# Kernel optimization log

Hardware: AMD Instinct MI355X
Metric: run time of the kernel (lower is better)

The kernel has to match this reference:

```python
import jax, jax.numpy as jnp
import numpy as np

N_NODES = 100000
N_EDGES = 1200000
DIM = 64


def _gcn_layer(h, src, dst, norm, W, b):
    # GCNConv: linear -> gather -> normalize -> scatter-add -> bias
    n = h.shape[0]
    h = h @ W                              # [N, D]
    msg = h[src] * norm[:, None]           # [E+N, D] gathered edge messages
    out = jax.ops.segment_sum(msg, dst, num_segments=n)
    return out + b


def setup_inputs() -> dict:
    key = jax.random.key(0)
    ks = jax.random.split(key, 8)
    s = 1.0 / np.sqrt(DIM)
    return {
        "x": jax.random.normal(ks[0], (N_NODES, DIM), jnp.float32),
        "edge_index": jax.random.randint(ks[1], (2, N_EDGES), 0, N_NODES, dtype=jnp.int32),
        "W1": jax.random.normal(ks[2], (DIM, DIM), jnp.float32) * s,
        "b1": jnp.zeros((DIM,), jnp.float32),
        "W2": jax.random.normal(ks[3], (DIM, DIM), jnp.float32) * s,
        "b2": jnp.zeros((DIM,), jnp.float32),
        "W3": jax.random.normal(ks[4], (DIM, DIM), jnp.float32) * s,
        "b3": jnp.zeros((DIM,), jnp.float32),
    }


def reference(x, edge_index, W1, b1, W2, b2, W3, b3):
    n = x.shape[0]
    loops = jnp.arange(n, dtype=edge_index.dtype)
    src = jnp.concatenate([edge_index[0], loops])   # add self-loops (PyG GCNConv default)
    dst = jnp.concatenate([edge_index[1], loops])
    # symmetric degree normalization: norm_e = d^-1/2[src] * d^-1/2[dst]
    deg = jax.ops.segment_sum(jnp.ones(src.shape, x.dtype), dst, num_segments=n)
    dinv = jnp.where(deg > 0, jax.lax.rsqrt(deg), 0.0)
    norm = dinv[src] * dinv[dst]
    h = jax.nn.relu(_gcn_layer(x, src, dst, norm, W1, b1))   # dropout inactive at eval
    h = jax.nn.relu(_gcn_layer(h, src, dst, norm, W2, b2))
    return _gcn_layer(h, src, dst, norm, W3, b3)
```

## Files before the change

### kernel.cpp

```cpp
#include <hip/hip_runtime.h>
#include <math.h>

#define N_NODES 100000
#define N_EDGES 1200000
#define DIM 64
#define ELL_STRIDE 48
#define BNODES 128
#define NBUCKET ((N_NODES + BNODES - 1) / BNODES)
#define BIN_SHIFT 10
#define NBIN ((N_NODES + 1023) >> 10)
#define BIN_CAP 16384
#define CAP 40
#define BIN_BLOCKS 512
#define EPB ((N_EDGES + BIN_BLOCKS - 1) / BIN_BLOCKS)
#define GEMM_BLOCKS ((N_NODES + 63) / 64)
#define GW_BLOCKS (N_NODES / 16)

#define PACK(s, dloc) (((unsigned)(dloc) << 17) | (unsigned)(s))
#define UNPACK_S(p)   ((int)((p) & 0x1FFFF))
#define UNPACK_D(p)   ((int)((p) >> 17))

typedef __attribute__((ext_vector_type(8))) short bf16x8;
typedef __attribute__((ext_vector_type(4))) float f32x4;

__device__ __forceinline__ unsigned short f2bf(float f) {
    union { float f; unsigned int u; } v; v.f = f;
    unsigned int r = v.u + 0x7FFF + ((v.u >> 16) & 1);
    return (unsigned short)(r >> 16);
}
__device__ __forceinline__ float bf2f(unsigned short us) {
    return __uint_as_float((unsigned int)us << 16);
}

#define LDH(boff) bf2f(*(const unsigned short*)((const char*)h + ((unsigned)(boff) + bo)))


__global__ void k_init(int* __restrict__ tail) {
    if (threadIdx.x < NBIN) tail[threadIdx.x * 16] = 0;
}


__device__ __forceinline__ void gemm_block(int bid, const float* __restrict__ x,
                                           const float* __restrict__ W,
                                           unsigned short* __restrict__ h,
                                           float4* __restrict__ Xlds) {
    const int tid = threadIdx.x;
    const int lane = tid & 63;

    float wreg[64];
#pragma unroll
    for (int k = 0; k < 64; ++k) wreg[k] = W[k * DIM + lane];

    const int base = bid * 64;
#pragma unroll
    for (int it = 0; it < 4; ++it) {
        int f = tid + it * 256;
        int row = base + (f >> 4);
        if (row >= N_NODES) row = N_NODES - 1;
        Xlds[f] = ((const float4*)x)[row * 16 + (f & 15)];
    }
    __syncthreads();

    const int m0 = (tid >> 6) * 16;
    for (int m = 0; m < 16; ++m) {
        const float4* xr = &Xlds[(m0 + m) * 16];
        float a0 = 0.f, a1 = 0.f, a2 = 0.f, a3 = 0.f;
#pragma unroll
        for (int k4 = 0; k4 < 16; ++k4) {
            float4 xv = xr[k4];
            a0 = fmaf(xv.x, wreg[k4 * 4 + 0], a0);
            a1 = fmaf(xv.y, wreg[k4 * 4 + 1], a1);
            a2 = fmaf(xv.z, wreg[k4 * 4 + 2], a2);
            a3 = fmaf(xv.w, wreg[k4 * 4 + 3], a3);
        }
        int row = base + m0 + m;
        if (row < N_NODES)
            h[(size_t)row * DIM + lane] = f2bf((a0 + a1) + (a2 + a3));
    }
}


__global__ void __launch_bounds__(256) k_pre(const int* __restrict__ ei,
                                             const float* __restrict__ x,
                                             const float* __restrict__ W1,
                                             int* __restrict__ tail,
                                             unsigned* __restrict__ part,
                                             unsigned short* __restrict__ h) {
    __shared__ __align__(16) char smraw[16384];
    __shared__ int lcnt[NBIN];
    __shared__ int gbase[NBIN];
    __shared__ int gcnt[NBIN];

    if (blockIdx.x < GEMM_BLOCKS) {
        gemm_block(blockIdx.x, x, W1, h, (float4*)smraw);
        return;
    }
    unsigned* stg = (unsigned*)smraw;
    const int tid = threadIdx.x;
    for (int i = tid; i < NBIN; i += 256) lcnt[i] = 0;
    __syncthreads();

    const int e0 = (blockIdx.x - GEMM_BLOCKS) * EPB;
    const int eend = (e0 + EPB < N_EDGES) ? e0 + EPB : N_EDGES;
    for (int e = e0 + tid; e < eend; e += 256) {
        int s = ei[e], d = ei[N_EDGES + e];
        int bin = d >> BIN_SHIFT;
        unsigned pk = PACK(s, d & 1023);
        int pos = atomicAdd(&lcnt[bin], 1);
        if (pos < CAP) {
            stg[bin * CAP + pos] = pk;
        } else {
            int gp = atomicAdd(&tail[bin * 16], 1);
            part[(size_t)bin * BIN_CAP + gp] = pk;
        }
    }
    __syncthreads();
    if (tid < NBIN) {
        int c = lcnt[tid]; if (c > CAP) c = CAP;
        gcnt[tid] = c;
        gbase[tid] = c ? atomicAdd(&tail[tid * 16], c) : 0;
    }
    __syncthreads();
    const int wv = tid >> 6, ln = tid & 63;
    for (int b = wv; b < NBIN; b += 4) {
        int c = gcnt[b];
        size_t gbb = (size_t)b * BIN_CAP + gbase[b];
        for (int i = ln; i < c; i += 64)
            part[gbb + i] = stg[b * CAP + i];
    }
}


__global__ void __launch_bounds__(256) k_bucket(const unsigned* __restrict__ part,
                                                const int* __restrict__ tail,
                                                int* __restrict__ ell,
                                                int* __restrict__ deg,
                                                unsigned short* __restrict__ hA,
                                                unsigned short* __restrict__ hB) {
    __shared__ int lcur[BNODES];
    __shared__ int lell[BNODES * ELL_STRIDE];
    const int bucket = blockIdx.x;
    const int tid = threadIdx.x;

    for (int i = tid; i < BNODES; i += 256) lcur[i] = 0;
    __syncthreads();

    const int bin = bucket >> 3;
    const int sub = bucket & 7;
    const int n = tail[bin * 16];
    const unsigned* pb = part + (size_t)bin * BIN_CAP;
    const int node0 = bucket * BNODES;
    for (int i = tid; i < n; i += 256) {
        unsigned p = pb[i];
        unsigned ld = (unsigned)(UNPACK_D(p) - (sub << 7));
        if (ld < BNODES) {
            int pos = atomicAdd(&lcur[ld], 1);
            if (pos < ELL_STRIDE) lell[ld * ELL_STRIDE + pos] = UNPACK_S(p) << 7;
        }
    }
    __syncthreads();

    for (int idx = tid; idx < BNODES * ELL_STRIDE; idx += 256) {
        int ln = idx / ELL_STRIDE, sl = idx - ln * ELL_STRIDE;
        int dg = lcur[ln];
        int pe = (dg + 7) & ~7;
        if (pe < 16) pe = 16;
        if (sl >= dg && sl < pe) lell[idx] = N_NODES << 7;
    }
    __syncthreads();

    int4* dst4 = (int4*)(ell + (size_t)bucket * BNODES * ELL_STRIDE);
    const int4* src4 = (const int4*)lell;
    for (int i = tid; i < BNODES * ELL_STRIDE / 4; i += 256) dst4[i] = src4[i];
    for (int i = tid; i < BNODES; i += 256) deg[node0 + i] = lcur[i];

    for (int i = tid; i < BNODES * 8; i += 256) {
        int ln = i >> 3;
        int node = node0 + ln;
        if (node < N_NODES) {
            float dd = rsqrtf((float)(lcur[ln] + 1));
            uint4* p = (uint4*)(hA + (size_t)node * DIM) + (i & 7);
            uint4 v = *p;
            float lo, hi;
            lo = __uint_as_float(v.x << 16) * dd; hi = __uint_as_float(v.x & 0xFFFF0000u) * dd;
            v.x = (unsigned)f2bf(lo) | ((unsigned)f2bf(hi) << 16);
            lo = __uint_as_float(v.y << 16) * dd; hi = __uint_as_float(v.y & 0xFFFF0000u) * dd;
            v.y = (unsigned)f2bf(lo) | ((unsigned)f2bf(hi) << 16);
            lo = __uint_as_float(v.z << 16) * dd; hi = __uint_as_float(v.z & 0xFFFF0000u) * dd;
            v.z = (unsigned)f2bf(lo) | ((unsigned)f2bf(hi) << 16);
            lo = __uint_as_float(v.w << 16) * dd; hi = __uint_as_float(v.w & 0xFFFF0000u) * dd;
            v.w = (unsigned)f2bf(lo) | ((unsigned)f2bf(hi) << 16);
            *p = v;
        }
    }
    if (bucket == 0) {
        if (tid < 8)  ((uint4*)(hA + (size_t)N_NODES * DIM))[tid] = make_uint4(0, 0, 0, 0);
        else if (tid < 16) ((uint4*)(hB + (size_t)N_NODES * DIM))[tid - 8] = make_uint4(0, 0, 0, 0);
    }
}


__global__ void __launch_bounds__(256, 4)
k_gatherW(const unsigned short* __restrict__ h,
          const int* __restrict__ deg,
          const int* __restrict__ ell,
          const float* __restrict__ bvec,
          const float* __restrict__ W,
          unsigned short* __restrict__ hout) {
    __shared__ unsigned short shb[2048];
    const int tid = threadIdx.x;
    const int lane = tid & 63;
    const int wv = tid >> 6;
    const int base = blockIdx.x * 16;
    const float bl = bvec[lane];
    const unsigned bo = 2u * (unsigned)lane;

#pragma unroll 2
    for (int m = 0; m < 4; ++m) {
        int node = base + wv * 4 + m;
        int dg = __builtin_amdgcn_readfirstlane(deg[node]);
        const int* row = ell + (size_t)node * ELL_STRIDE;

        int4 e0 = ((const int4*)row)[0];
        int4 e1 = ((const int4*)row)[1];
        int4 e2 = ((const int4*)row)[2];
        int4 e3 = ((const int4*)row)[3];
        float own = LDH((unsigned)node * 128u);

        float v0  = LDH(e0.x);
        float v1  = LDH(e0.y);
        float v2  = LDH(e0.z);
        float v3  = LDH(e0.w);
        float v4  = LDH(e1.x);
        float v5  = LDH(e1.y);
        float v6  = LDH(e1.z);
        float v7  = LDH(e1.w);
        float v8  = LDH(e2.x);
        float v9  = LDH(e2.y);
        float v10 = LDH(e2.z);
        float v11 = LDH(e2.w);
        float v12 = LDH(e3.x);
        float v13 = LDH(e3.y);
        float v14 = LDH(e3.z);
        float v15 = LDH(e3.w);

        float acc = ((own + v0) + (v1 + v2)) + ((v3 + v4) + (v5 + v6))
                  + ((v7 + v8) + (v9 + v10)) + ((v11 + v12) + ((v13 + v14) + v15));

        if (dg > 16) {
            int pe = (dg + 7) & ~7;
            for (int k = 16; k < pe; k += 8) {
                int4 a = *(const int4*)(row + k);
                int4 c = *(const int4*)(row + k + 4);
                float w0 = LDH(a.x);
                float w1 = LDH(a.y);
                float w2 = LDH(a.z);
                float w3 = LDH(a.w);
                float w4 = LDH(c.x);
                float w5 = LDH(c.y);
                float w6 = LDH(c.z);
                float w7 = LDH(c.w);
                acc += ((w0 + w1) + (w2 + w3)) + ((w4 + w5) + (w6 + w7));
            }
        }

        float dd = rsqrtf((float)(dg + 1));
        float o = fmaxf(fmaf(acc, dd, bl), 0.f);
        unsigned short oh = f2bf(o);
        unsigned short ol = f2bf(o - bf2f(oh));
        int r16 = wv * 4 + m;
        int pc = r16 * 64 + (((lane >> 3) ^ (r16 & 7)) << 3) + (lane & 7);
        shb[pc] = oh;
        shb[1024 + pc] = ol;
    }
    __syncthreads();

    const int bcol = wv * 16 + (lane & 15);
    const int g = lane >> 4;
    bf16x8 bh0, bl0, bh1, bl1;
#pragma unroll
    for (int j = 0; j < 8; ++j) {
        float w0 = W[(g * 8 + j) * DIM + bcol];
        float w1 = W[(g * 8 + j + 32) * DIM + bcol];
        unsigned short h0 = f2bf(w0);
        unsigned short h1 = f2bf(w1);
        bh0[j] = (short)h0; bl0[j] = (short)f2bf(w0 - bf2f(h0));
        bh1[j] = (short)h1; bl1[j] = (short)f2bf(w1 - bf2f(h1));
    }

    const int arow = lane & 15;
    const int cs = arow & 7;
    bf16x8 ah0 = *(const bf16x8*)&shb[arow * 64 + ((g ^ cs) << 3)];
    bf16x8 ah1 = *(const bf16x8*)&shb[arow * 64 + (((g + 4) ^ cs) << 3)];
    bf16x8 al0 = *(const bf16x8*)&shb[1024 + arow * 64 + ((g ^ cs) << 3)];
    bf16x8 al1 = *(const bf16x8*)&shb[1024 + arow * 64 + (((g + 4) ^ cs) << 3)];

    f32x4 acc = {0.f, 0.f, 0.f, 0.f};
    acc = __builtin_amdgcn_mfma_f32_16x16x32_bf16(ah0, bh0, acc, 0, 0, 0);
    acc = __builtin_amdgcn_mfma_f32_16x16x32_bf16(ah1, bh1, acc, 0, 0, 0);
    acc = __builtin_amdgcn_mfma_f32_16x16x32_bf16(al0, bh0, acc, 0, 0, 0);
    acc = __builtin_amdgcn_mfma_f32_16x16x32_bf16(al1, bh1, acc, 0, 0, 0);
    acc = __builtin_amdgcn_mfma_f32_16x16x32_bf16(ah0, bl0, acc, 0, 0, 0);
    acc = __builtin_amdgcn_mfma_f32_16x16x32_bf16(ah1, bl1, acc, 0, 0, 0);

#pragma unroll
    for (int r = 0; r < 4; ++r) {
        int rr = g * 4 + r;
        float res = acc[r] * rsqrtf((float)(deg[base + rr] + 1));
        hout[(size_t)(base + rr) * DIM + wv * 16 + (lane & 15)] = f2bf(res);
    }
}


__global__ void k_gatherF(const unsigned short* __restrict__ h,
                          const int* __restrict__ deg,
                          const int* __restrict__ ell, const float* __restrict__ b,
                          float* __restrict__ out) {
    int node = blockIdx.x * 4 + (threadIdx.x >> 6);
    const int lane = threadIdx.x & 63;
    const unsigned bo = 2u * (unsigned)lane;
    int dg = __builtin_amdgcn_readfirstlane(deg[node]);
    const int* row = ell + (size_t)node * ELL_STRIDE;

    int4 e0 = ((const int4*)row)[0];
    int4 e1 = ((const int4*)row)[1];
    int4 e2 = ((const int4*)row)[2];
    int4 e3 = ((const int4*)row)[3];
    float own = LDH((unsigned)node * 128u);

    float v0  = LDH(e0.x);
    float v1  = LDH(e0.y);
    float v2  = LDH(e0.z);
    float v3  = LDH(e0.w);
    float v4  = LDH(e1.x);
    float v5  = LDH(e1.y);
    float v6  = LDH(e1.z);
    float v7  = LDH(e1.w);
    float v8  = LDH(e2.x);
    float v9  = LDH(e2.y);
    float v10 = LDH(e2.z);
    float v11 = LDH(e2.w);
    float v12 = LDH(e3.x);
    float v13 = LDH(e3.y);
    float v14 = LDH(e3.z);
    float v15 = LDH(e3.w);

    float acc = ((own + v0) + (v1 + v2)) + ((v3 + v4) + (v5 + v6))
              + ((v7 + v8) + (v9 + v10)) + ((v11 + v12) + ((v13 + v14) + v15));

    if (dg > 16) {
        int pe = (dg + 7) & ~7;
        for (int k = 16; k < pe; k += 8) {
            int4 a = *(const int4*)(row + k);
            int4 c = *(const int4*)(row + k + 4);
            float w0 = LDH(a.x);
            float w1 = LDH(a.y);
            float w2 = LDH(a.z);
            float w3 = LDH(a.w);
            float w4 = LDH(c.x);
            float w5 = LDH(c.y);
            float w6 = LDH(c.z);
            float w7 = LDH(c.w);
            acc += ((w0 + w1) + (w2 + w3)) + ((w4 + w5) + (w6 + w7));
        }
    }

    float dd = rsqrtf((float)(dg + 1));
    out[(size_t)node * DIM + lane] = fmaf(acc, dd, b[lane]);
}


extern "C" void kernel_launch(void* const* d_in, const int* in_sizes, int n_in,
                              void* d_out, int out_size, void* d_ws, size_t ws_size,
                              hipStream_t stream) {
    const float* x   = (const float*)d_in[0];
    const int*   ei  = (const int*)d_in[1];
    const float* W1  = (const float*)d_in[2];
    const float* b1  = (const float*)d_in[3];
    const float* W2  = (const float*)d_in[4];
    const float* b2  = (const float*)d_in[5];
    const float* W3  = (const float*)d_in[6];
    const float* b3  = (const float*)d_in[7];
    float* out = (float*)d_out;

    char* ws = (char*)d_ws;
    int*            deg   = (int*)ws;
    int*            tailp = (int*)(ws + 0x70000);
    int*            ell   = (int*)(ws + 0xD00000);
    unsigned short* hbufA = (unsigned short*)(ws + 0x2000000);
    unsigned short* hbufB = (unsigned short*)(ws + 0x2D00000);
    unsigned*       part  = (unsigned*)(ws + 0x2D00000);

    k_init<<<1, 128, 0, stream>>>(tailp);

    k_pre<<<GEMM_BLOCKS + BIN_BLOCKS, 256, 0, stream>>>(ei, x, W1, tailp, part, hbufA);
    k_bucket<<<NBUCKET, 256, 0, stream>>>(part, tailp, ell, deg, hbufA, hbufB);

    k_gatherW<<<GW_BLOCKS, 256, 0, stream>>>(hbufA, deg, ell, b1, W2, hbufB);
    k_gatherW<<<GW_BLOCKS, 256, 0, stream>>>(hbufB, deg, ell, b2, W3, hbufA);
    k_gatherF<<<N_NODES / 4, 256, 0, stream>>>(hbufA, deg, ell, b3, out);
}
```

Baseline: 246.0 us.

## Compute first-layer GEMM with split-bf16 MFMA and replace init kernel with memset

The first-layer x@W1 projection inside k_pre now runs on MFMA 16x16x32 bf16 instructions instead of scalar FMAs with W held in registers. To keep near-fp32 accuracy, each operand is split into a high and a low bf16 part, giving three MFMA products per K chunk. Each block now handles 16 rows with no LDS staging, which means many more GEMM blocks in the fused launch. The tail-counter init kernel is replaced by hipMemsetAsync; the added precision-split arithmetic and a different error profile are the trade-offs.

```diff
diff --git a/kernel.cpp b/kernel.cpp
--- a/kernel.cpp
+++ b/kernel.cpp
@@ -13,7 +13,7 @@
 #define CAP 40
 #define BIN_BLOCKS 512
 #define EPB ((N_EDGES + BIN_BLOCKS - 1) / BIN_BLOCKS)
-#define GEMM_BLOCKS ((N_NODES + 63) / 64)
+#define GEMM1_BLOCKS (N_NODES / 16)
 #define GW_BLOCKS (N_NODES / 16)
 
 #define PACK(s, dloc) (((unsigned)(dloc) << 17) | (unsigned)(s))
@@ -34,49 +34,60 @@
 
 #define LDH(boff) bf2f(*(const unsigned short*)((const char*)h + ((unsigned)(boff) + bo)))
 
-
-__global__ void k_init(int* __restrict__ tail) {
-    if (threadIdx.x < NBIN) tail[threadIdx.x * 16] = 0;
-}
-
-
-__device__ __forceinline__ void gemm_block(int bid, const float* __restrict__ x,
-                                           const float* __restrict__ W,
-                                           unsigned short* __restrict__ h,
-                                           float4* __restrict__ Xlds) {
-    const int tid = threadIdx.x;
-    const int lane = tid & 63;
-
-    float wreg[64];
+__device__ __forceinline__ void split8(const float4 p, const float4 q,
+                                       bf16x8& hi, bf16x8& lo) {
+    float v[8] = {p.x, p.y, p.z, p.w, q.x, q.y, q.z, q.w};
 #pragma unroll
-    for (int k = 0; k < 64; ++k) wreg[k] = W[k * DIM + lane];
-
-    const int base = bid * 64;
+    for (int j = 0; j < 8; ++j) {
+        unsigned short h0 = f2bf(v[j]);
+        hi[j] = (short)h0;
+        lo[j] = (short)f2bf(v[j] - bf2f(h0));
+    }
+}
+
+
+__device__ __forceinline__ void gemm_block_mfma(int bid, const float* __restrict__ x,
+                                                const float* __restrict__ W,
+                                                unsigned short* __restrict__ h) {
+    const int lane = (int)(threadIdx.x & 63);
+    const int wv = (int)(threadIdx.x >> 6);
+    const int base = bid * 16;
+    const int g = lane >> 4;
+    const int r16 = lane & 15;
+
+    const float* xr = x + (size_t)(base + r16) * DIM + g * 8;
+    float4 a0 = *(const float4*)(xr);
+    float4 a1 = *(const float4*)(xr + 4);
+    float4 a2 = *(const float4*)(xr + 32);
+    float4 a3 = *(const float4*)(xr + 36);
+
+    bf16x8 ah0, al0, ah1, al1;
+    split8(a0, a1, ah0, al0);
+    split8(a2, a3, ah1, al1);
+
+    const int bcol = wv * 16 + r16;
+    bf16x8 bh0, bl0, bh1, bl1;
 #pragma unroll
-    for (int it = 0; it < 4; ++it) {
-        int f = tid + it * 256;
-        int row = base + (f >> 4);
-        if (row >= N_NODES) row = N_NODES - 1;
-        Xlds[f] = ((const float4*)x)[row * 16 + (f & 15)];
-    }
-    __syncthreads();
-
-    const int m0 = (tid >> 6) * 16;
-    for (int m = 0; m < 16; ++m) {
-        const float4* xr = &Xlds[(m0 + m) * 16];
-        float a0 = 0.f, a1 = 0.f, a2 = 0.f, a3 = 0.f;
+    for (int j = 0; j < 8; ++j) {
+        float w0 = W[(g * 8 + j) * DIM + bcol];
+        float w1 = W[(g * 8 + j + 32) * DIM + bcol];
+        unsigned short h0 = f2bf(w0);
+        unsigned short h1 = f2bf(w1);
+        bh0[j] = (short)h0; bl0[j] = (short)f2bf(w0 - bf2f(h0));
+        bh1[j] = (short)h1; bl1[j] = (short)f2bf(w1 - bf2f(h1));
+    }
+
+    f32x4 acc = {0.f, 0.f, 0.f, 0.f};
+    acc = __builtin_amdgcn_mfma_f32_16x16x32_bf16(ah0, bh0, acc, 0, 0, 0);
+    acc = __builtin_amdgcn_mfma_f32_16x16x32_bf16(ah1, bh1, acc, 0, 0, 0);
+    acc = __builtin_amdgcn_mfma_f32_16x16x32_bf16(al0, bh0, acc, 0, 0, 0);
+    acc = __builtin_amdgcn_mfma_f32_16x16x32_bf16(al1, bh1, acc, 0, 0, 0);
+    acc = __builtin_amdgcn_mfma_f32_16x16x32_bf16(ah0, bl0, acc, 0, 0, 0);
+    acc = __builtin_amdgcn_mfma_f32_16x16x32_bf16(ah1, bl1, acc, 0, 0, 0);
+
 #pragma unroll
-        for (int k4 = 0; k4 < 16; ++k4) {
-            float4 xv = xr[k4];
-            a0 = fmaf(xv.x, wreg[k4 * 4 + 0], a0);
-            a1 = fmaf(xv.y, wreg[k4 * 4 + 1], a1);
-            a2 = fmaf(xv.z, wreg[k4 * 4 + 2], a2);
-            a3 = fmaf(xv.w, wreg[k4 * 4 + 3], a3);
-        }
-        int row = base + m0 + m;
-        if (row < N_NODES)
-            h[(size_t)row * DIM + lane] = f2bf((a0 + a1) + (a2 + a3));
-    }
+    for (int r = 0; r < 4; ++r)
+        h[(size_t)(base + g * 4 + r) * DIM + bcol] = f2bf(acc[r]);
 }
 
 
@@ -86,21 +97,20 @@
                                              int* __restrict__ tail,
                                              unsigned* __restrict__ part,
                                              unsigned short* __restrict__ h) {
-    __shared__ __align__(16) char smraw[16384];
+    __shared__ unsigned stg[NBIN * CAP];
     __shared__ int lcnt[NBIN];
     __shared__ int gbase[NBIN];
     __shared__ int gcnt[NBIN];
 
-    if (blockIdx.x < GEMM_BLOCKS) {
-        gemm_block(blockIdx.x, x, W1, h, (float4*)smraw);
+    if (blockIdx.x < GEMM1_BLOCKS) {
+        gemm_block_mfma(blockIdx.x, x, W1, h);
         return;
     }
-    unsigned* stg = (unsigned*)smraw;
     const int tid = threadIdx.x;
     for (int i = tid; i < NBIN; i += 256) lcnt[i] = 0;
     __syncthreads();
 
-    const int e0 = (blockIdx.x - GEMM_BLOCKS) * EPB;
+    const int e0 = (blockIdx.x - GEMM1_BLOCKS) * EPB;
     const int eend = (e0 + EPB < N_EDGES) ? e0 + EPB : N_EDGES;
     for (int e = e0 + tid; e < eend; e += 256) {
         int s = ei[e], d = ei[N_EDGES + e];
@@ -391,9 +401,9 @@
     unsigned short* hbufB = (unsigned short*)(ws + 0x2D00000);
     unsigned*       part  = (unsigned*)(ws + 0x2D00000);
 
-    k_init<<<1, 128, 0, stream>>>(tailp);
-
-    k_pre<<<GEMM_BLOCKS + BIN_BLOCKS, 256, 0, stream>>>(ei, x, W1, tailp, part, hbufA);
+    hipMemsetAsync(tailp, 0, NBIN * 16 * sizeof(int), stream);
+
+    k_pre<<<GEMM1_BLOCKS + BIN_BLOCKS, 256, 0, stream>>>(ei, x, W1, tailp, part, hbufA);
     k_bucket<<<NBUCKET, 256, 0, stream>>>(part, tailp, ell, deg, hbufA, hbufB);
 
     k_gatherW<<<GW_BLOCKS, 256, 0, stream>>>(hbufA, deg, ell, b1, W2, hbufB);
```

After: 249.4 us. About the same (+1.4%).
